# Optimization experiments

Hardware: AMD Instinct MI355X
Metric: run time of the kernel (lower is better)

The kernel has to match this reference:

```python
import jax, jax.numpy as jnp
import numpy as np

B, L, E, H = 128, 256, 512, 512
S = 0.05  # weight scale


def setup_inputs() -> dict:
    key = jax.random.key(0)
    ks = jax.random.split(key, 12)
    return {
        "embedded_inputs": jax.random.normal(ks[0], (B, L, E), jnp.float32),
        "decoder_input": jax.random.normal(ks[1], (B, E), jnp.float32),
        "h0": jax.random.normal(ks[2], (B, H), jnp.float32),
        "c0": jax.random.normal(ks[3], (B, H), jnp.float32),
        "context": jax.random.normal(ks[4], (B, L, H), jnp.float32),
        "Wih": jax.random.normal(ks[5], (4 * H, E), jnp.float32) * S,
        "bih": jnp.zeros((4 * H,), jnp.float32),
        "Whh": jax.random.normal(ks[6], (4 * H, H), jnp.float32) * S,
        "bhh": jnp.zeros((4 * H,), jnp.float32),
        "Who": jax.random.normal(ks[7], (H, 2 * H), jnp.float32) * S,
        "bho": jnp.zeros((H,), jnp.float32),
        "Wa_in": jax.random.normal(ks[8], (H, H), jnp.float32) * S,
        "ba_in": jnp.zeros((H,), jnp.float32),
        "Wa_ctx": jax.random.normal(ks[9], (H, H), jnp.float32) * S,  # Conv1d(H,H,1) == per-position linear
        "ba_ctx": jnp.zeros((H,), jnp.float32),
        "V": jax.random.uniform(ks[10], (H,), jnp.float32, -1.0, 1.0),
    }


def reference(embedded_inputs, decoder_input, h0, c0, context,
              Wih, bih, Whh, bhh, Who, bho,
              Wa_in, ba_in, Wa_ctx, ba_ctx, V):
    Bsz, Ln, Ed = embedded_inputs.shape
    # context_linear (1x1 conv) depends only on context: precompute ctx [B,H,L]
    ctx = jnp.einsum('blh,oh->bol', context, Wa_ctx) + ba_ctx[None, :, None]
    mask0 = jnp.ones((Bsz, Ln), dtype=embedded_inputs.dtype)

    def step(carry, _):
        h, c, mask, dec_in = carry
        # LSTM cell gates
        gates = dec_in @ Wih.T + bih + h @ Whh.T + bhh  # [B,4H]
        ig, fg, gg, og = jnp.split(gates, 4, axis=1)
        c_t = jax.nn.sigmoid(fg) * c + jax.nn.sigmoid(ig) * jnp.tanh(gg)
        h_lstm = jax.nn.sigmoid(og) * jnp.tanh(c_t)
        # additive attention
        inp = h_lstm @ Wa_in.T + ba_in                     # [B,H]
        att = jnp.einsum('h,bhl->bl', V, jnp.tanh(inp[:, :, None] + ctx))
        att = jnp.where(mask == 0, -jnp.inf, att)
        alpha = jax.nn.softmax(att, axis=1)                # [B,L]
        hs = jnp.einsum('bhl,bl->bh', ctx, alpha)          # attention readout
        h_t = jnp.tanh(jnp.concatenate([hs, h_lstm], axis=1) @ Who.T + bho)
        # pointer selection + mask update
        idx = jnp.argmax(alpha * mask, axis=1)             # [B]
        onehot = jax.nn.one_hot(idx, Ln, dtype=mask.dtype)
        new_mask = mask * (1.0 - onehot)
        dec_next = jnp.take_along_axis(embedded_inputs, idx[:, None, None], axis=1)[:, 0, :]
        return (h_t, c_t, new_mask, dec_next), (alpha, idx)

    (hF, cF, _, _), (alphas, idxs) = jax.lax.scan(
        step, (h0, c0, mask0, decoder_input), None, length=Ln)
    outputs = jnp.transpose(alphas, (1, 0, 2))   # [B,L,L]
    pointers = jnp.transpose(idxs, (1, 0))       # [B,L]
    return outputs, pointers, hF, cF
```

## Files before the change

kernel.cpp:

```cpp
#include <hip/hip_runtime.h>
#include <math.h>

namespace {
constexpr int Bn = 128, Ln = 256, En = 512, Hn = 512;

constexpr long WS_CTX  = 8192;
constexpr long WS_H    = WS_CTX + (long)Bn * Ln * Hn;
constexpr long WS_C    = WS_H   + (long)Bn * Hn;
constexpr long WS_HL   = WS_C   + (long)Bn * Hn;
constexpr long WS_INP  = WS_HL  + (long)Bn * Hn;
constexpr long WS_HS   = WS_INP + (long)Bn * Hn;
constexpr long WS_DEC  = WS_HS  + (long)Bn * Hn;
constexpr long WS_ATT  = WS_DEC + (long)Bn * En;
constexpr long WS_MASK = WS_ATT + (long)Bn * Ln;

constexpr long OUT_PTR = (long)Bn * Ln * Ln;
constexpr long OUT_HF  = OUT_PTR + (long)Bn * Ln;
constexpr long OUT_CF  = OUT_HF + (long)Bn * Hn;
}

struct PParams {
  const float *emb, *dec0, *h0, *c0;
  const float *Wih, *bih, *Whh, *bhh;
  const float *Who, *bho, *Wa_in, *ba_in, *V;
  float *ws, *out;
};

__device__ __forceinline__ void gsync(unsigned* ub, unsigned target, int blk) {
  __syncthreads();
  unsigned* flags = ub;
  unsigned* gen   = ub + 4096;
  const int t = threadIdx.x;
  if (blk == 0) {
    for (;;) {
      unsigned v = (t > 0 && t < 256)
          ? __hip_atomic_load(&flags[t * 16], __ATOMIC_RELAXED, __HIP_MEMORY_SCOPE_AGENT)
          : target;
      int cnt = __syncthreads_count((int)(v >= target));
      if (cnt == (int)blockDim.x) break;
      __builtin_amdgcn_s_sleep(2);
    }
    __builtin_amdgcn_fence(__ATOMIC_ACQUIRE, "agent");
    if (t == 0)
      __hip_atomic_store(gen, target, __ATOMIC_RELEASE, __HIP_MEMORY_SCOPE_AGENT);
  } else {
    if (t == 0) {
      __hip_atomic_store(&flags[blk * 16], target, __ATOMIC_RELEASE, __HIP_MEMORY_SCOPE_AGENT);
      while (__hip_atomic_load(gen, __ATOMIC_RELAXED, __HIP_MEMORY_SCOPE_AGENT) < target)
        __builtin_amdgcn_s_sleep(2);
      (void)__hip_atomic_load(gen, __ATOMIC_ACQUIRE, __HIP_MEMORY_SCOPE_AGENT);
    }
  }
  __syncthreads();
}

__launch_bounds__(256)
__global__ void ctx_precompute(const float* __restrict__ context,
                               const float* __restrict__ Wa,
                               const float* __restrict__ ba,
                               float* __restrict__ ws) {
  __shared__ __align__(16) float As[16 * 68];
  __shared__ __align__(16) float Wsm[16 * 68];
  float* ctx = ws + WS_CTX;
  const int mt = blockIdx.x >> 3;
  const int nt = blockIdx.x & 7;
  const int t = threadIdx.x;
  const int tm = t & 15, tn = t >> 4;
  float acc00=0,acc01=0,acc02=0,acc03=0, acc10=0,acc11=0,acc12=0,acc13=0;
  float acc20=0,acc21=0,acc22=0,acc23=0, acc30=0,acc31=0,acc32=0,acc33=0;

  for (int kt = 0; kt < 32; ++kt) {
    __syncthreads();
    {
      const int m = t >> 2, k4 = t & 3;
      float4 a = *(const float4*)(context + (size_t)(mt * 64 + m) * 512 + kt * 16 + k4 * 4);
      As[(k4*4+0)*68 + m] = a.x; As[(k4*4+1)*68 + m] = a.y;
      As[(k4*4+2)*68 + m] = a.z; As[(k4*4+3)*68 + m] = a.w;
      float4 w = *(const float4*)(Wa + (size_t)(nt * 64 + m) * 512 + kt * 16 + k4 * 4);
      Wsm[(k4*4+0)*68 + m] = w.x; Wsm[(k4*4+1)*68 + m] = w.y;
      Wsm[(k4*4+2)*68 + m] = w.z; Wsm[(k4*4+3)*68 + m] = w.w;
    }
    __syncthreads();
#pragma unroll
    for (int k = 0; k < 16; ++k) {
      float4 a4 = *(const float4*)(As + k * 68 + tm * 4);
      float4 b4 = *(const float4*)(Wsm + k * 68 + tn * 4);
      acc00 = fmaf(a4.x, b4.x, acc00); acc01 = fmaf(a4.x, b4.y, acc01);
      acc02 = fmaf(a4.x, b4.z, acc02); acc03 = fmaf(a4.x, b4.w, acc03);
      acc10 = fmaf(a4.y, b4.x, acc10); acc11 = fmaf(a4.y, b4.y, acc11);
      acc12 = fmaf(a4.y, b4.z, acc12); acc13 = fmaf(a4.y, b4.w, acc13);
      acc20 = fmaf(a4.z, b4.x, acc20); acc21 = fmaf(a4.z, b4.y, acc21);
      acc22 = fmaf(a4.z, b4.z, acc22); acc23 = fmaf(a4.z, b4.w, acc23);
      acc30 = fmaf(a4.w, b4.x, acc30); acc31 = fmaf(a4.w, b4.y, acc31);
      acc32 = fmaf(a4.w, b4.z, acc32); acc33 = fmaf(a4.w, b4.w, acc33);
    }
  }
  const int col = nt * 64 + tn * 4;
  float4 bias = *(const float4*)(ba + col);
  float4 o0 = {acc00 + bias.x, acc01 + bias.y, acc02 + bias.z, acc03 + bias.w};
  float4 o1 = {acc10 + bias.x, acc11 + bias.y, acc12 + bias.z, acc13 + bias.w};
  float4 o2 = {acc20 + bias.x, acc21 + bias.y, acc22 + bias.z, acc23 + bias.w};
  float4 o3 = {acc30 + bias.x, acc31 + bias.y, acc32 + bias.z, acc33 + bias.w};
  const size_t base = (size_t)(mt * 64 + tm * 4) * 512 + col;
  *(float4*)(ctx + base + 0 * 512) = o0;
  *(float4*)(ctx + base + 1 * 512) = o1;
  *(float4*)(ctx + base + 2 * 512) = o2;
  *(float4*)(ctx + base + 3 * 512) = o3;
}

__launch_bounds__(1024, 4)
__global__ void pdecoder_main(PParams p) {
  __shared__ __align__(16) float smem[8192];

  float* ws = p.ws;
  unsigned* ub = (unsigned*)ws;
  unsigned tgt = 0;
  const int t = threadIdx.x, blk = blockIdx.x;

  float* ctx    = ws + WS_CTX;
  float* hbuf   = ws + WS_H;
  float* cbuf   = ws + WS_C;
  float* hlbuf  = ws + WS_HL;
  float* inpbuf = ws + WS_INP;
  float* hsbuf  = ws + WS_HS;
  float* decbuf = ws + WS_DEC;
  float* attbuf = ws + WS_ATT;
  float* maskbuf= ws + WS_MASK;

  {
    int idx = blk * 1024 + t;
    if (idx < Bn * Hn) { hbuf[idx] = p.h0[idx]; cbuf[idx] = p.c0[idx]; }
    if (idx < Bn * En) decbuf[idx] = p.dec0[idx];
    if (idx < Bn * Ln) maskbuf[idx] = 1.0f;
  }
  gsync(ub, ++tgt, blk);

  for (int step = 0; step < Ln; ++step) {
    {
      const int bt = blk >> 4, gt = blk & 15;
      const int bi = t & 7, cg = t >> 3;
      const int j0 = cg & 31, g = cg >> 5;
      const int gc = g * 512 + gt * 32 + j0;
      const int r = t >> 6, ks = t & 63;
      float4* Xs = (float4*)smem;
      float acc = 0.f;
      float4 pre;
      if (t < 512) pre = ((const float4*)(decbuf + (size_t)(bt * 8 + r) * 512))[ks];
#pragma unroll
      for (int kt = 0; kt < 4; ++kt) {
        __syncthreads();
        if (t < 512) Xs[r * 64 + (ks ^ r)] = pre;
        __syncthreads();
        if (t < 512 && kt < 3) {
          const float* src = (kt + 1 < 2) ? decbuf : hbuf;
          pre = ((const float4*)(src + (size_t)(bt * 8 + r) * 512 + ((kt + 1) & 1) * 256))[ks];
        }
        const float4* W4 = (const float4*)(((kt < 2) ? p.Wih : p.Whh) + (size_t)gc * 512 + (kt & 1) * 256);
#pragma unroll 8
        for (int k4 = 0; k4 < 64; ++k4) {
          float4 x = Xs[bi * 64 + (k4 ^ bi)];
          float4 w = W4[k4];
          acc = fmaf(x.x, w.x, acc); acc = fmaf(x.y, w.y, acc);
          acc = fmaf(x.z, w.z, acc); acc = fmaf(x.w, w.w, acc);
        }
      }
      __syncthreads();
      float* gs = smem + 4096;
      gs[bi * 132 + cg] = acc + p.bih[gc] + p.bhh[gc];
      __syncthreads();
      if (t < 256) {
        const int j = t & 31, bi2 = t >> 5;
        float ig = gs[bi2 * 132 + j];
        float fg = gs[bi2 * 132 + 32 + j];
        float gg = gs[bi2 * 132 + 64 + j];
        float og = gs[bi2 * 132 + 96 + j];
        const int b = bt * 8 + bi2, h = gt * 32 + j;
        float cold = cbuf[b * 512 + h];
        float is = 1.f / (1.f + expf(-ig));
        float fs = 1.f / (1.f + expf(-fg));
        float os = 1.f / (1.f + expf(-og));
        float ct = fs * cold + is * tanhf(gg);
        float hl = os * tanhf(ct);
        cbuf[b * 512 + h] = ct;
        hlbuf[b * 512 + h] = hl;
      }
    }
    gsync(ub, ++tgt, blk);

    {
      const int b = blk >> 1, oh = blk & 1;
      float* hl_s = smem;
      if (t < 128) ((float4*)hl_s)[t] = ((const float4*)(hlbuf + (size_t)b * 512))[t];
      __syncthreads();
      if (t < 256) {
        const int o = oh * 256 + t;
        const float4* xv = (const float4*)hl_s;
        const float4* Wr = (const float4*)(p.Wa_in + (size_t)o * 512);
        float acc = 0.f;
#pragma unroll 4
        for (int k4 = 0; k4 < 128; ++k4) {
          float4 x = xv[k4], w = Wr[k4];
          acc = fmaf(x.x, w.x, acc); acc = fmaf(x.y, w.y, acc);
          acc = fmaf(x.z, w.z, acc); acc = fmaf(x.w, w.w, acc);
        }
        inpbuf[b * 512 + o] = acc + p.ba_in[o];
      }
    }
    gsync(ub, ++tgt, blk);

    {
      const int b = blk >> 1, ph = blk & 1;
      float* inp_s = smem;
      float* V_s   = smem + 512;
      if (t < 512) { inp_s[t] = inpbuf[b * 512 + t]; V_s[t] = p.V[t]; }
      __syncthreads();
      const int w = t >> 6, lane = t & 63;
      const float4* inp4 = (const float4*)inp_s;
      const float4* V4   = (const float4*)V_s;
      float4 i0 = inp4[lane],  i1 = inp4[64 + lane];
      float4 v0 = V4[lane],    v1 = V4[64 + lane];
      for (int i = 0; i < 8; ++i) {
        const int l = ph * 128 + w * 8 + i;
        float msk = maskbuf[b * 256 + l];
        if (msk == 0.f) {
          if (lane == 0) attbuf[b * 256 + l] = -INFINITY;
          continue;
        }
        const float4* row = (const float4*)(ctx + (size_t)(b * 256 + l) * 512);
        float4 c0 = row[lane], c1 = row[64 + lane];
        float a;
        a = v0.x * tanhf(i0.x + c0.x);
        a = fmaf(v0.y, tanhf(i0.y + c0.y), a);
        a = fmaf(v0.z, tanhf(i0.z + c0.z), a);
        a = fmaf(v0.w, tanhf(i0.w + c0.w), a);
        a = fmaf(v1.x, tanhf(i1.x + c1.x), a);
        a = fmaf(v1.y, tanhf(i1.y + c1.y), a);
        a = fmaf(v1.z, tanhf(i1.z + c1.z), a);
        a = fmaf(v1.w, tanhf(i1.w + c1.w), a);
#pragma unroll
        for (int off = 32; off > 0; off >>= 1) a += __shfl_xor(a, off, 64);
        if (lane == 0) attbuf[b * 256 + l] = a;
      }
    }
    gsync(ub, ++tgt, blk);

    {
      const int b = blk >> 1, ph = blk & 1;
      float* att_s   = smem;
      float* val_s   = smem + 256;
      int*   idx_s   = (int*)(smem + 512);
      float* alpha_s = smem + 768;
      float* part_s  = smem + 1024;
      if (t < 256) {
        float a = attbuf[b * 256 + t];
        att_s[t] = a; val_s[t] = a; idx_s[t] = t;
      }
      __syncthreads();
      for (int s = 128; s > 0; s >>= 1) {
        if (t < s) {
          float v1 = val_s[t], v2 = val_s[t + s];
          int   i1 = idx_s[t], i2 = idx_s[t + s];
          if (v2 > v1 || (v2 == v1 && i2 < i1)) { val_s[t] = v2; idx_s[t] = i2; }
        }
        __syncthreads();
      }
      const float m = val_s[0];
      const int am = idx_s[0];
      __syncthreads();
      if (t < 256) {
        float e = expf(att_s[t] - m);
        alpha_s[t] = e; val_s[t] = e;
      }
      __syncthreads();
      for (int s = 128; s > 0; s >>= 1) {
        if (t < s) val_s[t] += val_s[t + s];
        __syncthreads();
      }
      const float Z = val_s[0];
      __syncthreads();
      if (t < 256) alpha_s[t] = alpha_s[t] / Z;
      __syncthreads();
      if (ph == 0) {
        if (t < 256) p.out[(size_t)b * Ln * Ln + (size_t)step * Ln + t] = alpha_s[t];
        if (t == 0) {
          p.out[OUT_PTR + (size_t)b * Ln + step] = (float)am;
          maskbuf[b * 256 + am] = 0.f;
        }
        if (t < 512) decbuf[b * 512 + t] = p.emb[((size_t)(b * 256) + am) * 512 + t];
      }
      const int hi = t & 255, lp = (t >> 8) & 1;
      const int h = ph * 256 + hi;
      float acc = 0.f;
      if (t < 512) {
        const float* cb = ctx + (size_t)b * 256 * 512 + h;
#pragma unroll 4
        for (int l = lp * 128; l < lp * 128 + 128; ++l) {
          float al = alpha_s[l];
          if (al != 0.f) acc = fmaf(al, cb[(size_t)l * 512], acc);
        }
      }
      if (t < 512 && lp == 1) part_s[hi] = acc;
      __syncthreads();
      if (t < 512 && lp == 0) hsbuf[(size_t)b * 512 + h] = acc + part_s[hi];
    }
    gsync(ub, ++tgt, blk);

    {
      const int b = blk >> 1, oh = blk & 1;
      float* hs_s  = smem;
      float* hl_s  = smem + 512;
      float* partF = smem + 1024;
      if (t < 128) {
        ((float4*)hs_s)[t] = ((const float4*)(hsbuf + (size_t)b * 512))[t];
        ((float4*)hl_s)[t] = ((const float4*)(hlbuf + (size_t)b * 512))[t];
      }
      __syncthreads();
      float acc = 0.f;
      if (t < 512) {
        const int oj = t & 255, kh = t >> 8;
        const int o = oh * 256 + oj;
        const float4* xv = (const float4*)(kh ? hl_s : hs_s);
        const float4* Wr = (const float4*)(p.Who + (size_t)o * 1024 + (size_t)kh * 512);
#pragma unroll 4
        for (int k4 = 0; k4 < 128; ++k4) {
          float4 x = xv[k4], w = Wr[k4];
          acc = fmaf(x.x, w.x, acc); acc = fmaf(x.y, w.y, acc);
          acc = fmaf(x.z, w.z, acc); acc = fmaf(x.w, w.w, acc);
        }
        if (kh == 1) partF[oj] = acc;
      }
      __syncthreads();
      if (t < 256) {
        const int o = oh * 256 + t;
        hbuf[(size_t)b * 512 + o] = tanhf(acc + partF[t] + p.bho[o]);
      }
    }
    gsync(ub, ++tgt, blk);
  }

  {
    int idx = blk * 1024 + t;
    if (idx < Bn * Hn) {
      p.out[OUT_HF + idx] = hbuf[idx];
      p.out[OUT_CF + idx] = cbuf[idx];
    }
  }
}

extern "C" void kernel_launch(void* const* d_in, const int* in_sizes, int n_in,
                              void* d_out, int out_size, void* d_ws, size_t ws_size,
                              hipStream_t stream) {
  (void)in_sizes; (void)n_in; (void)out_size; (void)ws_size;
  const float* emb     = (const float*)d_in[0];
  const float* dec0    = (const float*)d_in[1];
  const float* h0      = (const float*)d_in[2];
  const float* c0      = (const float*)d_in[3];
  const float* context = (const float*)d_in[4];
  const float* Wih     = (const float*)d_in[5];
  const float* bih     = (const float*)d_in[6];
  const float* Whh     = (const float*)d_in[7];
  const float* bhh     = (const float*)d_in[8];
  const float* Who     = (const float*)d_in[9];
  const float* bho     = (const float*)d_in[10];
  const float* Wa_in   = (const float*)d_in[11];
  const float* ba_in   = (const float*)d_in[12];
  const float* Wa_ctx  = (const float*)d_in[13];
  const float* ba_ctx  = (const float*)d_in[14];
  const float* V       = (const float*)d_in[15];
  float* ws  = (float*)d_ws;
  float* out = (float*)d_out;

  hipMemsetAsync(d_ws, 0, 32768, stream);

  hipLaunchKernelGGL(ctx_precompute, dim3(4096), dim3(256), 0, stream,
                     context, Wa_ctx, ba_ctx, ws);

  PParams prm{emb, dec0, h0, c0, Wih, bih, Whh, bhh, Who, bho, Wa_in, ba_in, V, ws, out};
  void* args[] = {&prm};
  hipLaunchCooperativeKernel((const void*)pdecoder_main, dim3(256), dim3(1024),
                             args, 0, stream);
}
```

Before: 43.94 ms.

## Fuse attention and output stages to remove two grid barriers per decode step

The Wa_in projection is merged into the attention-score stage, and the attention readout is merged into the Who output projection, so each decode step needs three grid-wide barriers instead of five. The inpbuf/hsbuf global buffers go away. To make this work, each block of a batch pair now computes the full 512-wide projection and the full context readout redundantly, which doubles the Wa_in and ctx reads for those parts. The attention loop also prefetches the next ctx row and reads the mask with vector loads. A leftover line reads the uninitialised 'os' before it is reassigned.

```diff
diff --git a/kernel.cpp b/kernel.cpp
--- a/kernel.cpp
+++ b/kernel.cpp
@@ -8,9 +8,7 @@
 constexpr long WS_H    = WS_CTX + (long)Bn * Ln * Hn;
 constexpr long WS_C    = WS_H   + (long)Bn * Hn;
 constexpr long WS_HL   = WS_C   + (long)Bn * Hn;
-constexpr long WS_INP  = WS_HL  + (long)Bn * Hn;
-constexpr long WS_HS   = WS_INP + (long)Bn * Hn;
-constexpr long WS_DEC  = WS_HS  + (long)Bn * Hn;
+constexpr long WS_DEC  = WS_HL  + (long)Bn * Hn;
 constexpr long WS_ATT  = WS_DEC + (long)Bn * En;
 constexpr long WS_MASK = WS_ATT + (long)Bn * Ln;
 
@@ -121,8 +119,6 @@
   float* hbuf   = ws + WS_H;
   float* cbuf   = ws + WS_C;
   float* hlbuf  = ws + WS_HL;
-  float* inpbuf = ws + WS_INP;
-  float* hsbuf  = ws + WS_HS;
   float* decbuf = ws + WS_DEC;
   float* attbuf = ws + WS_ATT;
   float* maskbuf= ws + WS_MASK;
@@ -178,7 +174,9 @@
         float cold = cbuf[b * 512 + h];
         float is = 1.f / (1.f + expf(-ig));
         float fs = 1.f / (1.f + expf(-fg));
-        float os = 1.f / (1.f + expf(-og));
+        float os = 1.f / (1.f + expf(-os * 0.f + og));
+        (void)os;
+        os = 1.f / (1.f + expf(-og));
         float ct = fs * cold + is * tanhf(gg);
         float hl = os * tanhf(ct);
         cbuf[b * 512 + h] = ct;
@@ -188,14 +186,16 @@
     gsync(ub, ++tgt, blk);
 
     {
-      const int b = blk >> 1, oh = blk & 1;
-      float* hl_s = smem;
+      const int b = blk >> 1, ph = blk & 1;
+      float* hl_s  = smem;
+      float* inp_s = smem + 512;
+      float* V_s   = smem + 1024;
       if (t < 128) ((float4*)hl_s)[t] = ((const float4*)(hlbuf + (size_t)b * 512))[t];
-      __syncthreads();
-      if (t < 256) {
-        const int o = oh * 256 + t;
+      if (t >= 128 && t < 256) ((float4*)V_s)[t - 128] = ((const float4*)p.V)[t - 128];
+      __syncthreads();
+      if (t < 512) {
         const float4* xv = (const float4*)hl_s;
-        const float4* Wr = (const float4*)(p.Wa_in + (size_t)o * 512);
+        const float4* Wr = (const float4*)(p.Wa_in + (size_t)t * 512);
         float acc = 0.f;
 #pragma unroll 4
         for (int k4 = 0; k4 < 128; ++k4) {
@@ -203,43 +203,50 @@
           acc = fmaf(x.x, w.x, acc); acc = fmaf(x.y, w.y, acc);
           acc = fmaf(x.z, w.z, acc); acc = fmaf(x.w, w.w, acc);
         }
-        inpbuf[b * 512 + o] = acc + p.ba_in[o];
-      }
-    }
-    gsync(ub, ++tgt, blk);
-
-    {
-      const int b = blk >> 1, ph = blk & 1;
-      float* inp_s = smem;
-      float* V_s   = smem + 512;
-      if (t < 512) { inp_s[t] = inpbuf[b * 512 + t]; V_s[t] = p.V[t]; }
-      __syncthreads();
-      const int w = t >> 6, lane = t & 63;
-      const float4* inp4 = (const float4*)inp_s;
-      const float4* V4   = (const float4*)V_s;
-      float4 i0 = inp4[lane],  i1 = inp4[64 + lane];
-      float4 v0 = V4[lane],    v1 = V4[64 + lane];
-      for (int i = 0; i < 8; ++i) {
-        const int l = ph * 128 + w * 8 + i;
-        float msk = maskbuf[b * 256 + l];
-        if (msk == 0.f) {
-          if (lane == 0) attbuf[b * 256 + l] = -INFINITY;
-          continue;
-        }
-        const float4* row = (const float4*)(ctx + (size_t)(b * 256 + l) * 512);
+        inp_s[t] = acc + p.ba_in[t];
+      }
+      __syncthreads();
+      {
+        const int w = t >> 6, lane = t & 63;
+        const float4* inp4 = (const float4*)inp_s;
+        const float4* V4   = (const float4*)V_s;
+        float4 i0 = inp4[lane],  i1 = inp4[64 + lane];
+        float4 v0 = V4[lane],    v1 = V4[64 + lane];
+        const int l0 = ph * 128 + w * 8;
+        float4 m01 = *(const float4*)(maskbuf + b * 256 + l0);
+        float4 m23 = *(const float4*)(maskbuf + b * 256 + l0 + 4);
+        const float mk0 = m01.x, mk1 = m01.y, mk2 = m01.z, mk3 = m01.w;
+        const float mk4 = m23.x, mk5 = m23.y, mk6 = m23.z, mk7 = m23.w;
+        const float4* row = (const float4*)(ctx + (size_t)(b * 256 + l0) * 512);
         float4 c0 = row[lane], c1 = row[64 + lane];
-        float a;
-        a = v0.x * tanhf(i0.x + c0.x);
-        a = fmaf(v0.y, tanhf(i0.y + c0.y), a);
-        a = fmaf(v0.z, tanhf(i0.z + c0.z), a);
-        a = fmaf(v0.w, tanhf(i0.w + c0.w), a);
-        a = fmaf(v1.x, tanhf(i1.x + c1.x), a);
-        a = fmaf(v1.y, tanhf(i1.y + c1.y), a);
-        a = fmaf(v1.z, tanhf(i1.z + c1.z), a);
-        a = fmaf(v1.w, tanhf(i1.w + c1.w), a);
 #pragma unroll
-        for (int off = 32; off > 0; off >>= 1) a += __shfl_xor(a, off, 64);
-        if (lane == 0) attbuf[b * 256 + l] = a;
+        for (int i = 0; i < 8; ++i) {
+          const float msk = (i == 0) ? mk0 : (i == 1) ? mk1 : (i == 2) ? mk2 :
+                            (i == 3) ? mk3 : (i == 4) ? mk4 : (i == 5) ? mk5 :
+                            (i == 6) ? mk6 : mk7;
+          float4 cc0 = c0, cc1 = c1;
+          if (i < 7) {
+            const float4* nr = row + (size_t)(i + 1) * 128;
+            c0 = nr[lane]; c1 = nr[64 + lane];
+          }
+          const int l = l0 + i;
+          if (msk != 0.f) {
+            float a;
+            a = v0.x * tanhf(i0.x + cc0.x);
+            a = fmaf(v0.y, tanhf(i0.y + cc0.y), a);
+            a = fmaf(v0.z, tanhf(i0.z + cc0.z), a);
+            a = fmaf(v0.w, tanhf(i0.w + cc0.w), a);
+            a = fmaf(v1.x, tanhf(i1.x + cc1.x), a);
+            a = fmaf(v1.y, tanhf(i1.y + cc1.y), a);
+            a = fmaf(v1.z, tanhf(i1.z + cc1.z), a);
+            a = fmaf(v1.w, tanhf(i1.w + cc1.w), a);
+#pragma unroll
+            for (int off = 32; off > 0; off >>= 1) a += __shfl_xor(a, off, 64);
+            if (lane == 0) attbuf[b * 256 + l] = a;
+          } else {
+            if (lane == 0) attbuf[b * 256 + l] = -INFINITY;
+          }
+        }
       }
     }
     gsync(ub, ++tgt, blk);
@@ -251,10 +258,15 @@
       int*   idx_s   = (int*)(smem + 512);
       float* alpha_s = smem + 768;
       float* part_s  = smem + 1024;
+      float* hs_s    = smem + 1536;
+      float* hl_s    = smem + 2048;
+      float* partF   = smem + 2560;
       if (t < 256) {
         float a = attbuf[b * 256 + t];
         att_s[t] = a; val_s[t] = a; idx_s[t] = t;
       }
+      if (t >= 512 && t < 640)
+        ((float4*)hl_s)[t - 512] = ((const float4*)(hlbuf + (size_t)b * 512))[t - 512];
       __syncthreads();
       for (int s = 128; s > 0; s >>= 1) {
         if (t < s) {
@@ -288,51 +300,36 @@
         }
         if (t < 512) decbuf[b * 512 + t] = p.emb[((size_t)(b * 256) + am) * 512 + t];
       }
-      const int hi = t & 255, lp = (t >> 8) & 1;
-      const int h = ph * 256 + hi;
-      float acc = 0.f;
-      if (t < 512) {
+      {
+        const int h = t & 511, lp = t >> 9;
+        float acc = 0.f;
         const float* cb = ctx + (size_t)b * 256 * 512 + h;
-#pragma unroll 4
-        for (int l = lp * 128; l < lp * 128 + 128; ++l) {
-          float al = alpha_s[l];
-          if (al != 0.f) acc = fmaf(al, cb[(size_t)l * 512], acc);
-        }
-      }
-      if (t < 512 && lp == 1) part_s[hi] = acc;
-      __syncthreads();
-      if (t < 512 && lp == 0) hsbuf[(size_t)b * 512 + h] = acc + part_s[hi];
-    }
-    gsync(ub, ++tgt, blk);
-
-    {
-      const int b = blk >> 1, oh = blk & 1;
-      float* hs_s  = smem;
-      float* hl_s  = smem + 512;
-      float* partF = smem + 1024;
-      if (t < 128) {
-        ((float4*)hs_s)[t] = ((const float4*)(hsbuf + (size_t)b * 512))[t];
-        ((float4*)hl_s)[t] = ((const float4*)(hlbuf + (size_t)b * 512))[t];
-      }
-      __syncthreads();
-      float acc = 0.f;
+#pragma unroll 8
+        for (int l = lp * 128; l < lp * 128 + 128; ++l)
+          acc = fmaf(alpha_s[l], cb[(size_t)l * 512], acc);
+        if (lp == 1) part_s[h] = acc;
+        __syncthreads();
+        if (lp == 0) hs_s[h] = acc + part_s[h];
+      }
+      __syncthreads();
+      float accF = 0.f;
       if (t < 512) {
         const int oj = t & 255, kh = t >> 8;
-        const int o = oh * 256 + oj;
+        const int o = ph * 256 + oj;
         const float4* xv = (const float4*)(kh ? hl_s : hs_s);
         const float4* Wr = (const float4*)(p.Who + (size_t)o * 1024 + (size_t)kh * 512);
 #pragma unroll 4
         for (int k4 = 0; k4 < 128; ++k4) {
           float4 x = xv[k4], w = Wr[k4];
-          acc = fmaf(x.x, w.x, acc); acc = fmaf(x.y, w.y, acc);
-          acc = fmaf(x.z, w.z, acc); acc = fmaf(x.w, w.w, acc);
-        }
-        if (kh == 1) partF[oj] = acc;
+          accF = fmaf(x.x, w.x, accF); accF = fmaf(x.y, w.y, accF);
+          accF = fmaf(x.z, w.z, accF); accF = fmaf(x.w, w.w, accF);
+        }
+        if (kh == 1) partF[oj] = accF;
       }
       __syncthreads();
       if (t < 256) {
-        const int o = oh * 256 + t;
-        hbuf[(size_t)b * 512 + o] = tanhf(acc + partF[t] + p.bho[o]);
+        const int o = ph * 256 + t;
+        hbuf[(size_t)b * 512 + o] = tanhf(accF + partF[t] + p.bho[o]);
       }
     }
     gsync(ub, ++tgt, blk);
```

After: 44.73 ms. Within noise of the previous version (+1.8%).

## Transpose attention/output weights for coalesced GEMV and compact nonzero alpha indices

Applied to the files above, without the earlier changes.

Adds a pre-kernel that transposes Wa_in and Who into the workspace, so per-step GEMVs read weight columns with lanes hitting consecutive addresses instead of each thread striding its own row. The attention readout now builds a compacted list of nonzero alpha positions via a prefix scan and only gathers those ctx rows, in unrolled batches of eight. The gate GEMV unroll is also raised. In exchange it adds extra workspace, a launch, and several extra block barriers per step for the scan.

```diff
diff --git a/kernel.cpp b/kernel.cpp
--- a/kernel.cpp
+++ b/kernel.cpp
@@ -13,6 +13,8 @@
 constexpr long WS_DEC  = WS_HS  + (long)Bn * Hn;
 constexpr long WS_ATT  = WS_DEC + (long)Bn * En;
 constexpr long WS_MASK = WS_ATT + (long)Bn * Ln;
+constexpr long WS_WTA  = WS_MASK + (long)Bn * Ln;
+constexpr long WS_WTO  = WS_WTA + (long)512 * 512;
 
 constexpr long OUT_PTR = (long)Bn * Ln * Ln;
 constexpr long OUT_HF  = OUT_PTR + (long)Bn * Ln;
@@ -108,6 +110,29 @@
   *(float4*)(ctx + base + 3 * 512) = o3;
 }
 
+__launch_bounds__(256)
+__global__ void transpose_w(const float* __restrict__ Wa_in,
+                            const float* __restrict__ Who,
+                            float* __restrict__ ws) {
+  __shared__ float tile[64][65];
+  const int bid = blockIdx.x, t = threadIdx.x;
+  const float* src; float* dst; int K, rt, ct;
+  if (bid < 64) { src = Wa_in; dst = ws + WS_WTA; K = 512;  rt = bid >> 3;        ct = bid & 7;  }
+  else          { src = Who;   dst = ws + WS_WTO; K = 1024; rt = (bid - 64) >> 4; ct = (bid - 64) & 15; }
+  const int lr = t >> 6, lc = t & 63;
+#pragma unroll
+  for (int i = 0; i < 16; ++i) {
+    int r = i * 4 + lr;
+    tile[r][lc] = src[(size_t)(rt * 64 + r) * K + ct * 64 + lc];
+  }
+  __syncthreads();
+#pragma unroll
+  for (int i = 0; i < 16; ++i) {
+    int r = i * 4 + lr;
+    dst[(size_t)(ct * 64 + r) * 512 + rt * 64 + lc] = tile[lc][r];
+  }
+}
+
 __launch_bounds__(1024, 4)
 __global__ void pdecoder_main(PParams p) {
   __shared__ __align__(16) float smem[8192];
@@ -126,6 +151,8 @@
   float* decbuf = ws + WS_DEC;
   float* attbuf = ws + WS_ATT;
   float* maskbuf= ws + WS_MASK;
+  const float* WTA = ws + WS_WTA;
+  const float* WTO = ws + WS_WTO;
 
   {
     int idx = blk * 1024 + t;
@@ -156,7 +183,7 @@
           pre = ((const float4*)(src + (size_t)(bt * 8 + r) * 512 + ((kt + 1) & 1) * 256))[ks];
         }
         const float4* W4 = (const float4*)(((kt < 2) ? p.Wih : p.Whh) + (size_t)gc * 512 + (kt & 1) * 256);
-#pragma unroll 8
+#pragma unroll 16
         for (int k4 = 0; k4 < 64; ++k4) {
           float4 x = Xs[bi * 64 + (k4 ^ bi)];
           float4 w = W4[k4];
@@ -194,15 +221,11 @@
       __syncthreads();
       if (t < 256) {
         const int o = oh * 256 + t;
-        const float4* xv = (const float4*)hl_s;
-        const float4* Wr = (const float4*)(p.Wa_in + (size_t)o * 512);
+        const float* Wc = WTA + o;
         float acc = 0.f;
-#pragma unroll 4
-        for (int k4 = 0; k4 < 128; ++k4) {
-          float4 x = xv[k4], w = Wr[k4];
-          acc = fmaf(x.x, w.x, acc); acc = fmaf(x.y, w.y, acc);
-          acc = fmaf(x.z, w.z, acc); acc = fmaf(x.w, w.w, acc);
-        }
+#pragma unroll 32
+        for (int k = 0; k < 512; ++k)
+          acc = fmaf(hl_s[k], Wc[(size_t)k * 512], acc);
         inpbuf[b * 512 + o] = acc + p.ba_in[o];
       }
     }
@@ -288,15 +311,43 @@
         }
         if (t < 512) decbuf[b * 512 + t] = p.emb[((size_t)(b * 256) + am) * 512 + t];
       }
+      if (t < 256) att_s[t] = (alpha_s[t] != 0.f) ? 1.f : 0.f;
+      __syncthreads();
+      for (int s = 1; s < 256; s <<= 1) {
+        float add = 0.f;
+        if (t < 256 && t >= s) add = att_s[t - s];
+        __syncthreads();
+        if (t < 256) att_s[t] += add;
+        __syncthreads();
+      }
+      if (t < 256 && alpha_s[t] != 0.f) idx_s[(int)att_s[t] - 1] = t;
+      __syncthreads();
+      const int cnt0 = (int)att_s[127];
+      const int cntA = (int)att_s[255];
       const int hi = t & 255, lp = (t >> 8) & 1;
       const int h = ph * 256 + hi;
       float acc = 0.f;
       if (t < 512) {
         const float* cb = ctx + (size_t)b * 256 * 512 + h;
-#pragma unroll 4
-        for (int l = lp * 128; l < lp * 128 + 128; ++l) {
-          float al = alpha_s[l];
-          if (al != 0.f) acc = fmaf(al, cb[(size_t)l * 512], acc);
+        int j = lp ? cnt0 : 0;
+        const int jhi = lp ? cntA : cnt0;
+        for (; j + 8 <= jhi; j += 8) {
+          int l0 = idx_s[j+0], l1 = idx_s[j+1], l2 = idx_s[j+2], l3 = idx_s[j+3];
+          int l4 = idx_s[j+4], l5 = idx_s[j+5], l6 = idx_s[j+6], l7 = idx_s[j+7];
+          float a0 = alpha_s[l0], a1 = alpha_s[l1], a2 = alpha_s[l2], a3 = alpha_s[l3];
+          float a4 = alpha_s[l4], a5 = alpha_s[l5], a6 = alpha_s[l6], a7 = alpha_s[l7];
+          float c0 = cb[(size_t)l0 * 512], c1 = cb[(size_t)l1 * 512];
+          float c2 = cb[(size_t)l2 * 512], c3 = cb[(size_t)l3 * 512];
+          float c4 = cb[(size_t)l4 * 512], c5 = cb[(size_t)l5 * 512];
+          float c6 = cb[(size_t)l6 * 512], c7 = cb[(size_t)l7 * 512];
+          acc = fmaf(a0, c0, acc); acc = fmaf(a1, c1, acc);
+          acc = fmaf(a2, c2, acc); acc = fmaf(a3, c3, acc);
+          acc = fmaf(a4, c4, acc); acc = fmaf(a5, c5, acc);
+          acc = fmaf(a6, c6, acc); acc = fmaf(a7, c7, acc);
+        }
+        for (; j < jhi; ++j) {
+          int l = idx_s[j];
+          acc = fmaf(alpha_s[l], cb[(size_t)l * 512], acc);
         }
       }
       if (t < 512 && lp == 1) part_s[hi] = acc;
@@ -319,14 +370,11 @@
       if (t < 512) {
         const int oj = t & 255, kh = t >> 8;
         const int o = oh * 256 + oj;
-        const float4* xv = (const float4*)(kh ? hl_s : hs_s);
-        const float4* Wr = (const float4*)(p.Who + (size_t)o * 1024 + (size_t)kh * 512);
-#pragma unroll 4
-        for (int k4 = 0; k4 < 128; ++k4) {
-          float4 x = xv[k4], w = Wr[k4];
-          acc = fmaf(x.x, w.x, acc); acc = fmaf(x.y, w.y, acc);
-          acc = fmaf(x.z, w.z, acc); acc = fmaf(x.w, w.w, acc);
-        }
+        const float* xv = kh ? hl_s : hs_s;
+        const float* Wc = WTO + (size_t)kh * 512 * 512 + o;
+#pragma unroll 32
+        for (int k = 0; k < 512; ++k)
+          acc = fmaf(xv[k], Wc[(size_t)k * 512], acc);
         if (kh == 1) partF[oj] = acc;
       }
       __syncthreads();
@@ -374,6 +422,8 @@
 
   hipLaunchKernelGGL(ctx_precompute, dim3(4096), dim3(256), 0, stream,
                      context, Wa_ctx, ba_ctx, ws);
+  hipLaunchKernelGGL(transpose_w, dim3(192), dim3(256), 0, stream,
+                     Wa_in, Who, ws);
 
   PParams prm{emb, dec0, h0, c0, Wih, bih, Whh, bhh, Who, bho, Wa_in, ba_in, V, ws, out};
   void* args[] = {&prm};
```

New measurement: 85.91 ms. 95.5% more time.
